# Kernel tuning notes

Hardware: AMD Instinct MI355X
Metric: run time of the kernel (lower is better)

Reference implementation:

```python
import jax, jax.numpy as jnp
import numpy as np

D_MODEL = 1024
N_HEADS = 16
N_KV_HEADS = 4
HEAD_DIM = D_MODEL // N_HEADS
NUM_REP = N_HEADS // N_KV_HEADS
B, T = 2, 2048


def setup_inputs() -> dict:
    key = jax.random.key(0)
    ks = jax.random.split(key, 9)
    s = 0.02
    x = jax.random.normal(ks[0], (B, T, D_MODEL), dtype=jnp.float32)
    # causal mask: True = masked (matches torch masked_fill semantics)
    mask = jnp.triu(jnp.ones((T, T), dtype=bool), k=1)[None, None]
    kv_dim = N_KV_HEADS * HEAD_DIM
    return {
        "x": x,
        "mask": mask,
        "Wq": jax.random.normal(ks[1], (D_MODEL, D_MODEL), jnp.float32) * s,
        "bq": jnp.zeros((D_MODEL,), jnp.float32),
        "Wk": jax.random.normal(ks[2], (D_MODEL, kv_dim), jnp.float32) * s,
        "bk": jnp.zeros((kv_dim,), jnp.float32),
        "Wv": jax.random.normal(ks[3], (D_MODEL, kv_dim), jnp.float32) * s,
        "bv": jnp.zeros((kv_dim,), jnp.float32),
        "Wo": jax.random.normal(ks[4], (D_MODEL, D_MODEL), jnp.float32) * s,
        "bo": jnp.zeros((D_MODEL,), jnp.float32),
    }


def reference(x, mask, Wq, bq, Wk, bk, Wv, bv, Wo, bo):
    Bx, Tx, C = x.shape
    # projections
    q = (x @ Wq + bq).reshape(Bx, Tx, N_HEADS, HEAD_DIM).transpose(0, 2, 1, 3)  # (B,H,T,D)
    k = (x @ Wk + bk).reshape(Bx, Tx, N_KV_HEADS, HEAD_DIM)
    v = (x @ Wv + bv).reshape(Bx, Tx, N_KV_HEADS, HEAD_DIM)
    # repeat_kv: expand+reshape == repeat along head axis
    k = jnp.repeat(k, NUM_REP, axis=2).transpose(0, 2, 1, 3)  # (B,H,T,D)
    v = jnp.repeat(v, NUM_REP, axis=2).transpose(0, 2, 1, 3)
    scale = 1.0 / jnp.sqrt(jnp.asarray(HEAD_DIM, x.dtype))
    attn = jnp.einsum('bhtd,bhsd->bhts', q, k) * scale  # (B,H,T,T)
    attn = jnp.where(mask, -jnp.inf, attn)
    attn = jax.nn.softmax(attn, axis=-1)
    out = jnp.einsum('bhts,bhsd->bhtd', attn, v)
    out = out.transpose(0, 2, 1, 3).reshape(Bx, Tx, C)
    return out @ Wo + bo
```

## Files before the change

kernel.cpp:

```cpp
#include <hip/hip_runtime.h>
#include <hip/hip_bf16.h>
#include <cmath>
#include <stdint.h>


typedef __attribute__((ext_vector_type(4))) float f32x4;
typedef __attribute__((ext_vector_type(16))) float f32x16;
typedef __attribute__((ext_vector_type(8))) short s16x8;
typedef __attribute__((ext_vector_type(8))) unsigned short u16x8;

#define MFMA32(a, b, c) __builtin_amdgcn_mfma_f32_32x32x16_bf16(a, b, c, 0, 0, 0)

__device__ __forceinline__ unsigned short f2bf(float f) {
    unsigned int u = __float_as_uint(f);
    u += 0x7FFFu + ((u >> 16) & 1u);
    return (unsigned short)(u >> 16);
}

__device__ __forceinline__ unsigned int pktr(float lo, float hi) {
    return __builtin_amdgcn_perm(__float_as_uint(hi), __float_as_uint(lo), 0x07060302u);
}

__device__ __forceinline__ void async16(void* lds, const void* g) {
    __builtin_amdgcn_global_load_lds(
        (const __attribute__((address_space(1))) unsigned int*)g,
        (__attribute__((address_space(3))) unsigned int*)lds, 16, 0, 0);
}

__global__ __launch_bounds__(256) void prep(
        const float* __restrict__ x,
        const float* __restrict__ Wq, const float* __restrict__ Wk,
        const float* __restrict__ Wv, const float* __restrict__ Wo,
        const float* __restrict__ bq, const float* __restrict__ bk,
        const float* __restrict__ bv,
        unsigned short* __restrict__ xb, unsigned short* __restrict__ Wqkv,
        unsigned short* __restrict__ Wot, float* __restrict__ biasq, float qscale) {
    __shared__ unsigned short sx[128 * 72];
    __shared__ float tile[32][33];
    const int bid = blockIdx.x, tid = threadIdx.x;
    if (bid < 512) {
        const int mt = bid >> 4, kt = bid & 15;
#pragma unroll
        for (int i = 0; i < 8; ++i) {
            const int flat = (i * 256 + tid) * 4;
            const int row = flat >> 6, col = flat & 63;
            f32x4 ld = *reinterpret_cast<const f32x4*>(
                &x[(size_t)(mt * 128 + row) * 1024 + kt * 64 + col]);
            unsigned short* d = &sx[row * 72 + col];
            d[0] = f2bf(ld.x); d[1] = f2bf(ld.y); d[2] = f2bf(ld.z); d[3] = f2bf(ld.w);
        }
        __syncthreads();
#pragma unroll
        for (int j = 0; j < 4; ++j) {
            const int idx = j * 256 + tid;
            const int kb = idx >> 7, m = idx & 127;
            u16x8 v = *reinterpret_cast<const u16x8*>(&sx[m * 72 + kb * 8]);
            *reinterpret_cast<u16x8*>(
                &xb[(size_t)(((mt * 16 + kt) * 8 + kb) * 128 + m) * 8]) = v;
        }
    } else if (bid < 3072) {
        int id = bid - 512;
        const float* W; unsigned short* out; int N, nbase; float scale = 1.0f;
        if (id < 1024)      { W = Wq; out = Wqkv; N = 1024; nbase = 0;    scale = qscale; }
        else if (id < 1280) { W = Wk; out = Wqkv; N = 256;  nbase = 1024; id -= 1024; }
        else if (id < 1536) { W = Wv; out = Wqkv; N = 256;  nbase = 1280; id -= 1280; }
        else                { W = Wo; out = Wot;  N = 1024; nbase = 0;    id -= 1536; }
        const int nb = N >> 5;
        const int n0 = (id % nb) * 32, k0 = (id / nb) * 32;
        const int tx = tid & 31, ty = tid >> 5;
#pragma unroll
        for (int r = 0; r < 4; ++r)
            tile[ty + r * 8][tx] = W[(size_t)(k0 + ty + r * 8) * N + n0 + tx];
        __syncthreads();
        const int k = k0 + tx;
#pragma unroll
        for (int r = 0; r < 4; ++r) {
            const int n = nbase + n0 + ty + r * 8;
            size_t addr = (size_t)((n >> 6) * 16 + (k >> 6)) * 4096
                        + (size_t)((((k >> 3) & 7) * 64 + (n & 63)) * 8 + (k & 7));
            out[addr] = f2bf(tile[tx][ty + r * 8] * scale);
        }
    } else {
        const int i = (bid - 3072) * 256 + tid;
        if (i < 1024) biasq[i] = bq[i] * qscale;
        else if (i < 1280) biasq[i] = bk[i - 1024];
        else biasq[i] = bv[i - 1280];
    }
}

template <int EPI>
__global__ __launch_bounds__(256) void gemm_mn(
        const unsigned short* __restrict__ A, const unsigned short* __restrict__ Bt,
        const float* __restrict__ bias,
        unsigned short* __restrict__ oQ, unsigned short* __restrict__ oK,
        unsigned short* __restrict__ oV, float* __restrict__ oF) {
    __shared__ alignas(16) unsigned short smem[24576];
    const int tid = threadIdx.x;
    const int lane = tid & 63, w = tid >> 6;
    const int l31 = lane & 31, grp = lane >> 5;
    const int m0 = blockIdx.y * 128, n0 = blockIdx.x * 64;
    const int wm = w * 32;

    const unsigned short* Abase = A + (size_t)blockIdx.y * (16 * 8192) + (size_t)tid * 8;
    const unsigned short* Bbase = Bt + (size_t)blockIdx.x * (16 * 4096) + (size_t)tid * 8;

    f32x16 acc0 = {}, acc1 = {};

#pragma unroll
    for (int i = 0; i < 4; ++i)
        async16(&smem[(size_t)(i * 256 + (tid & 192)) * 8], Abase + (size_t)i * 2048);
#pragma unroll
    for (int i = 0; i < 2; ++i)
        async16(&smem[16384 + (size_t)(i * 256 + (tid & 192)) * 8], Bbase + (size_t)i * 2048);

    for (int kt = 0; kt < 16; ++kt) {
        const int cur = kt & 1;
        unsigned short* cA = smem + cur * 8192;
        unsigned short* cB = smem + 16384 + cur * 4096;
        __syncthreads();
        if (kt < 15) {
            unsigned short* nA = smem + (cur ^ 1) * 8192;
            unsigned short* nB = smem + 16384 + (cur ^ 1) * 4096;
            const unsigned short* ab = Abase + (size_t)(kt + 1) * 8192;
            const unsigned short* bb = Bbase + (size_t)(kt + 1) * 4096;
#pragma unroll
            for (int i = 0; i < 4; ++i)
                async16(&nA[(size_t)(i * 256 + (tid & 192)) * 8], ab + (size_t)i * 2048);
#pragma unroll
            for (int i = 0; i < 2; ++i)
                async16(&nB[(size_t)(i * 256 + (tid & 192)) * 8], bb + (size_t)i * 2048);
        }
#pragma unroll
        for (int kc = 0; kc < 4; ++kc) {
            const int kb = kc * 2 + grp;
            s16x8 a  = *reinterpret_cast<const s16x8*>(&cA[(size_t)(kb * 128 + wm + l31) * 8]);
            s16x8 b0 = *reinterpret_cast<const s16x8*>(&cB[(size_t)(kb * 64 + l31) * 8]);
            s16x8 b1 = *reinterpret_cast<const s16x8*>(&cB[(size_t)(kb * 64 + 32 + l31) * 8]);
            acc0 = MFMA32(a, b0, acc0);
            acc1 = MFMA32(a, b1, acc1);
        }
    }
    const float bv0 = bias[n0 + l31], bv1 = bias[n0 + 32 + l31];
    if (EPI == 0 && n0 >= 1280) {
        __syncthreads();
#pragma unroll
        for (int r = 0; r < 16; ++r) {
            const int m = wm + (r & 3) + 8 * (r >> 2) + 4 * grp;
            smem[(size_t)l31 * 136 + m] = f2bf(acc0[r] + bv0);
            smem[(size_t)(l31 + 32) * 136 + m] = f2bf(acc1[r] + bv1);
        }
        __syncthreads();
#pragma unroll
        for (int i = 0; i < 4; ++i) {
            const int id = i * 256 + tid;
            const int n = id >> 4, mc = id & 15;
            u16x8 v = *reinterpret_cast<const u16x8*>(&smem[(size_t)n * 136 + mc * 8]);
            *reinterpret_cast<u16x8*>(&oV[(size_t)(n0 - 1280 + n) * 4096 + m0 + mc * 8]) = v;
        }
        return;
    }
#pragma unroll
    for (int r = 0; r < 16; ++r) {
        const int row = m0 + wm + (r & 3) + 8 * (r >> 2) + 4 * grp;
        const float v0 = acc0[r] + bv0, v1 = acc1[r] + bv1;
        if (EPI == 0) {
            if (n0 < 1024) {
                oQ[(size_t)row * 1024 + n0 + l31] = f2bf(v0);
                oQ[(size_t)row * 1024 + n0 + 32 + l31] = f2bf(v1);
            } else {
                oK[(size_t)row * 256 + (n0 - 1024) + l31] = f2bf(v0);
                oK[(size_t)row * 256 + (n0 - 1024) + 32 + l31] = f2bf(v1);
            }
        } else {
            oF[(size_t)row * 1024 + n0 + l31] = v0;
            oF[(size_t)row * 1024 + n0 + 32 + l31] = v1;
        }
    }
}

__global__ __launch_bounds__(512) void flash_attn(
        const unsigned short* __restrict__ Qb, const unsigned short* __restrict__ Kb,
        const unsigned short* __restrict__ Vt, unsigned short* __restrict__ Ot) {
    __shared__ alignas(16) unsigned short sK[2][64 * 72];
    __shared__ alignas(16) unsigned short sV[2][64 * 72];
    const int tid = threadIdx.x;
    const int lane = tid & 63, w = tid >> 6;
    const int ln = lane & 31, grp = lane >> 5;
    const int bh = blockIdx.x;
    const int qp = blockIdx.y;
    const int b = bh >> 4, h = bh & 15, kvh = h >> 2;
    const int myqt = (w < 4) ? qp : (15 - qp);
    const int nch_mine = 2 * myqt + 2;
    const int nch_all = 32 - 2 * qp;
    const int t0w = myqt * 128 + (w & 3) * 32;
    const int qrow_g = t0w + ln;

    const unsigned short* Qrow = Qb + (size_t)(b * 2048 + qrow_g) * 1024 + h * 64;
    s16x8 qf[4];
#pragma unroll
    for (int kk = 0; kk < 4; ++kk)
        qf[kk] = *reinterpret_cast<const s16x8*>(Qrow + kk * 16 + grp * 8);

    const unsigned short* Kbase = Kb + (size_t)(b * 2048) * 256 + kvh * 64;
    const unsigned short* Vbase = Vt + (size_t)(kvh * 64) * 4096 + (size_t)b * 2048;

    const int srow = tid >> 3, sd0 = (tid & 7) * 8;
    u16x8 kreg = *reinterpret_cast<const u16x8*>(Kbase + (size_t)srow * 256 + sd0);
    u16x8 vreg = *reinterpret_cast<const u16x8*>(Vbase + (size_t)srow * 4096 + sd0);

    f32x16 o0 = {}, o1 = {};
    float ltot = 0.f;
    s16x8 pfv[4];
    s16x8 vp0[4], vp1[4];

    for (int c = 0; c < nch_all; ++c) {
        unsigned short* bK = sK[c & 1];
        unsigned short* bV = sV[c & 1];
        *reinterpret_cast<u16x8*>(&bK[srow * 72 + sd0]) = kreg;
        *reinterpret_cast<u16x8*>(&bV[srow * 72 + sd0]) = vreg;
        __syncthreads();
        if (c + 1 < nch_all) {
            const int s1 = (c + 1) * 64;
            kreg = *reinterpret_cast<const u16x8*>(Kbase + (size_t)(s1 + srow) * 256 + sd0);
            vreg = *reinterpret_cast<const u16x8*>(Vbase + (size_t)srow * 4096 + s1 + sd0);
        }
        if (c >= 1 && c <= nch_mine) {
#pragma unroll
            for (int kkp = 0; kkp < 4; ++kkp) {
                o0 = MFMA32(pfv[kkp], vp0[kkp], o0);
                o1 = MFMA32(pfv[kkp], vp1[kkp], o1);
            }
        }
        if (c < nch_mine) {
            const int s0 = c * 64;
#pragma unroll
            for (int kkp = 0; kkp < 4; ++kkp) {
                vp0[kkp] = *reinterpret_cast<const s16x8*>(&bV[ln * 72 + kkp * 16 + grp * 8]);
                vp1[kkp] = *reinterpret_cast<const s16x8*>(&bV[(32 + ln) * 72 + kkp * 16 + grp * 8]);
            }
            f32x16 st0 = {}, st1 = {};
#pragma unroll
            for (int kk = 0; kk < 4; ++kk) {
                s16x8 k0 = *reinterpret_cast<const s16x8*>(&bK[ln * 72 + kk * 16 + grp * 8]);
                s16x8 k1 = *reinterpret_cast<const s16x8*>(&bK[(32 + ln) * 72 + kk * 16 + grp * 8]);
                st0 = MFMA32(k0, qf[kk], st0);
                st1 = MFMA32(k1, qf[kk], st1);
            }
            if (s0 + 63 > t0w) {
#pragma unroll
                for (int r = 0; r < 16; ++r) {
                    const int keyo = s0 + (r & 3) + 8 * (r >> 2) + 4 * grp;
                    if (keyo > qrow_g)      st0[r] = -INFINITY;
                    if (keyo + 32 > qrow_g) st1[r] = -INFINITY;
                }
            }
            f32x16 p0, p1;
#pragma unroll
            for (int r = 0; r < 16; ++r) {
                p0[r] = __builtin_amdgcn_exp2f(st0[r]);
                p1[r] = __builtin_amdgcn_exp2f(st1[r]);
            }
            float a0 = 0.f, a1 = 0.f, a2 = 0.f, a3 = 0.f;
#pragma unroll
            for (int r = 0; r < 16; r += 2) {
                a0 += p0[r]; a1 += p0[r + 1];
                a2 += p1[r]; a3 += p1[r + 1];
            }
            ltot += (a0 + a1) + (a2 + a3);
#pragma unroll
            for (int kkp = 0; kkp < 4; ++kkp) {
                const f32x16& pm = (kkp < 2) ? p0 : p1;
                const int A4 = 8 * (kkp & 1);
                unsigned int pA0 = pktr(pm[A4 + 0], pm[A4 + 1]);
                unsigned int pA1 = pktr(pm[A4 + 2], pm[A4 + 3]);
                unsigned int pB0 = pktr(pm[A4 + 4], pm[A4 + 5]);
                unsigned int pB1 = pktr(pm[A4 + 6], pm[A4 + 7]);
                unsigned int x0 = (unsigned int)__shfl_xor((int)(grp ? pA0 : pB0), 32, 64);
                unsigned int x1 = (unsigned int)__shfl_xor((int)(grp ? pA1 : pB1), 32, 64);
                union { unsigned int u[4]; s16x8 v; } pf;
                pf.u[0] = grp ? x0 : pA0;
                pf.u[1] = grp ? x1 : pA1;
                pf.u[2] = grp ? pB0 : x0;
                pf.u[3] = grp ? pB1 : x1;
                pfv[kkp] = pf.v;
            }
        }
    }
    if (w >= 4) {
#pragma unroll
        for (int kkp = 0; kkp < 4; ++kkp) {
            o0 = MFMA32(pfv[kkp], vp0[kkp], o0);
            o1 = MFMA32(pfv[kkp], vp1[kkp], o1);
        }
    }

    const float lfull = ltot + __shfl_xor(ltot, 32, 64);
    const float rl = 1.0f / lfull;
    unsigned short* Otb = Ot + (size_t)((b * 16 + myqt) * 16 + h) * 8192
                             + (size_t)(ln >> 3) * 1024 + (ln & 7);
#pragma unroll
    for (int r = 0; r < 16; ++r) {
        const int row = (r & 3) + 8 * (r >> 2) + 4 * grp;
        const float rr = __shfl(rl, row, 64);
        const size_t off = (size_t)((w & 3) * 32 + row) * 8;
        Otb[off]        = f2bf(o0[r] * rr);
        Otb[off + 4096] = f2bf(o1[r] * rr);
    }
}

extern "C" void kernel_launch(void* const* d_in, const int* in_sizes, int n_in,
                              void* d_out, int out_size, void* d_ws, size_t ws_size,
                              hipStream_t stream) {
    const float* x  = (const float*)d_in[0];
    const float* Wq = (const float*)d_in[2];
    const float* bq = (const float*)d_in[3];
    const float* Wk = (const float*)d_in[4];
    const float* bk = (const float*)d_in[5];
    const float* Wv = (const float*)d_in[6];
    const float* bv = (const float*)d_in[7];
    const float* Wo = (const float*)d_in[8];
    const float* bo = (const float*)d_in[9];
    float* out = (float*)d_out;

    char* ws = (char*)d_ws;
    unsigned short* xb    = (unsigned short*)(ws);
    unsigned short* Wqkv  = (unsigned short*)(ws + (8u  << 20));
    unsigned short* Wot   = (unsigned short*)(ws + (12u << 20));
    float*          biasq = (float*)         (ws + (15u << 20));
    unsigned short* Qb    = (unsigned short*)(ws + (16u << 20));
    unsigned short* Kb    = (unsigned short*)(ws + (24u << 20));
    unsigned short* Vtp   = (unsigned short*)(ws + (26u << 20));
    unsigned short* Otl   = (unsigned short*)(ws + (28u << 20));

    const float qscale = 0.125f * 1.4426950408889634f;

    prep<<<3078, 256, 0, stream>>>(x, Wq, Wk, Wv, Wo, bq, bk, bv,
                                   xb, Wqkv, Wot, biasq, qscale);
    gemm_mn<0><<<dim3(24, 32), 256, 0, stream>>>(xb, Wqkv, biasq, Qb, Kb, Vtp, nullptr);
    flash_attn<<<dim3(32, 8), 512, 0, stream>>>(Qb, Kb, Vtp, Otl);
    gemm_mn<1><<<dim3(16, 32), 256, 0, stream>>>(Otl, Wot, bo, nullptr, nullptr, nullptr, out);
}
```

Before: 168.7 us.

## Split flash attention into single-wave blocks reading K/V directly from global

Replaces the 512-thread flash attention block, which staged K/V tiles through double-buffered LDS with barriers, with 2048 single-wavefront blocks. Each block handles one 32-row query strip and loads K and V fragments straight from global memory into registers. Strips are launched longest-first, and the block index is ordered so that the four query heads sharing a KV head run close together for L2 reuse. This removes LDS traffic and __syncthreads and allows finer load balancing. The cost is that K/V reuse across waves in a block is lost, raising global/L2 load traffic, and there is no software prefetch overlapping loads with compute.

```diff
diff --git a/kernel.cpp b/kernel.cpp
--- a/kernel.cpp
+++ b/kernel.cpp
@@ -178,22 +178,19 @@
     }
 }
 
-__global__ __launch_bounds__(512) void flash_attn(
+__global__ __launch_bounds__(64) void flash_attn(
         const unsigned short* __restrict__ Qb, const unsigned short* __restrict__ Kb,
         const unsigned short* __restrict__ Vt, unsigned short* __restrict__ Ot) {
-    __shared__ alignas(16) unsigned short sK[2][64 * 72];
-    __shared__ alignas(16) unsigned short sV[2][64 * 72];
-    const int tid = threadIdx.x;
-    const int lane = tid & 63, w = tid >> 6;
+    const int lane = threadIdx.x;
     const int ln = lane & 31, grp = lane >> 5;
-    const int bh = blockIdx.x;
-    const int qp = blockIdx.y;
-    const int b = bh >> 4, h = bh & 15, kvh = h >> 2;
-    const int myqt = (w < 4) ? qp : (15 - qp);
-    const int nch_mine = 2 * myqt + 2;
-    const int nch_all = 32 - 2 * qp;
-    const int t0w = myqt * 128 + (w & 3) * 32;
+    const int id = blockIdx.x;
+    const int kvh = id & 3;
+    const int b = (id >> 2) & 1;
+    const int h = kvh * 4 + ((id >> 3) & 3);
+    const int strip = 63 - (id >> 5);
+    const int t0w = strip * 32;
     const int qrow_g = t0w + ln;
+    const int nch = (strip >> 1) + 1;
 
     const unsigned short* Qrow = Qb + (size_t)(b * 2048 + qrow_g) * 1024 + h * 64;
     s16x8 qf[4];
@@ -201,108 +198,82 @@
     for (int kk = 0; kk < 4; ++kk)
         qf[kk] = *reinterpret_cast<const s16x8*>(Qrow + kk * 16 + grp * 8);
 
-    const unsigned short* Kbase = Kb + (size_t)(b * 2048) * 256 + kvh * 64;
-    const unsigned short* Vbase = Vt + (size_t)(kvh * 64) * 4096 + (size_t)b * 2048;
-
-    const int srow = tid >> 3, sd0 = (tid & 7) * 8;
-    u16x8 kreg = *reinterpret_cast<const u16x8*>(Kbase + (size_t)srow * 256 + sd0);
-    u16x8 vreg = *reinterpret_cast<const u16x8*>(Vbase + (size_t)srow * 4096 + sd0);
+    const unsigned short* Kp = Kb + (size_t)(b * 2048) * 256 + kvh * 64;
+    const unsigned short* Vp = Vt + (size_t)(kvh * 64) * 4096 + (size_t)b * 2048;
+    const unsigned short* kr0 = Kp + (size_t)ln * 256 + grp * 8;
+    const unsigned short* kr1 = Kp + (size_t)(32 + ln) * 256 + grp * 8;
+    const unsigned short* vr0 = Vp + (size_t)ln * 4096 + grp * 8;
+    const unsigned short* vr1 = Vp + (size_t)(32 + ln) * 4096 + grp * 8;
 
     f32x16 o0 = {}, o1 = {};
     float ltot = 0.f;
-    s16x8 pfv[4];
-    s16x8 vp0[4], vp1[4];
-
-    for (int c = 0; c < nch_all; ++c) {
-        unsigned short* bK = sK[c & 1];
-        unsigned short* bV = sV[c & 1];
-        *reinterpret_cast<u16x8*>(&bK[srow * 72 + sd0]) = kreg;
-        *reinterpret_cast<u16x8*>(&bV[srow * 72 + sd0]) = vreg;
-        __syncthreads();
-        if (c + 1 < nch_all) {
-            const int s1 = (c + 1) * 64;
-            kreg = *reinterpret_cast<const u16x8*>(Kbase + (size_t)(s1 + srow) * 256 + sd0);
-            vreg = *reinterpret_cast<const u16x8*>(Vbase + (size_t)srow * 4096 + s1 + sd0);
-        }
-        if (c >= 1 && c <= nch_mine) {
-#pragma unroll
-            for (int kkp = 0; kkp < 4; ++kkp) {
-                o0 = MFMA32(pfv[kkp], vp0[kkp], o0);
-                o1 = MFMA32(pfv[kkp], vp1[kkp], o1);
+
+    for (int c = 0; c < nch; ++c) {
+        const int s0 = c * 64;
+        s16x8 kf0[4], kf1[4], vf0[4], vf1[4];
+#pragma unroll
+        for (int kk = 0; kk < 4; ++kk) {
+            kf0[kk] = *reinterpret_cast<const s16x8*>(kr0 + (size_t)s0 * 256 + kk * 16);
+            kf1[kk] = *reinterpret_cast<const s16x8*>(kr1 + (size_t)s0 * 256 + kk * 16);
+            vf0[kk] = *reinterpret_cast<const s16x8*>(vr0 + s0 + kk * 16);
+            vf1[kk] = *reinterpret_cast<const s16x8*>(vr1 + s0 + kk * 16);
+        }
+        f32x16 st0 = {}, st1 = {};
+#pragma unroll
+        for (int kk = 0; kk < 4; ++kk) {
+            st0 = MFMA32(kf0[kk], qf[kk], st0);
+            st1 = MFMA32(kf1[kk], qf[kk], st1);
+        }
+        if (s0 + 63 > t0w) {
+#pragma unroll
+            for (int r = 0; r < 16; ++r) {
+                const int keyo = s0 + (r & 3) + 8 * (r >> 2) + 4 * grp;
+                if (keyo > qrow_g)      st0[r] = -INFINITY;
+                if (keyo + 32 > qrow_g) st1[r] = -INFINITY;
             }
         }
-        if (c < nch_mine) {
-            const int s0 = c * 64;
-#pragma unroll
-            for (int kkp = 0; kkp < 4; ++kkp) {
-                vp0[kkp] = *reinterpret_cast<const s16x8*>(&bV[ln * 72 + kkp * 16 + grp * 8]);
-                vp1[kkp] = *reinterpret_cast<const s16x8*>(&bV[(32 + ln) * 72 + kkp * 16 + grp * 8]);
-            }
-            f32x16 st0 = {}, st1 = {};
-#pragma unroll
-            for (int kk = 0; kk < 4; ++kk) {
-                s16x8 k0 = *reinterpret_cast<const s16x8*>(&bK[ln * 72 + kk * 16 + grp * 8]);
-                s16x8 k1 = *reinterpret_cast<const s16x8*>(&bK[(32 + ln) * 72 + kk * 16 + grp * 8]);
-                st0 = MFMA32(k0, qf[kk], st0);
-                st1 = MFMA32(k1, qf[kk], st1);
-            }
-            if (s0 + 63 > t0w) {
-#pragma unroll
-                for (int r = 0; r < 16; ++r) {
-                    const int keyo = s0 + (r & 3) + 8 * (r >> 2) + 4 * grp;
-                    if (keyo > qrow_g)      st0[r] = -INFINITY;
-                    if (keyo + 32 > qrow_g) st1[r] = -INFINITY;
-                }
-            }
-            f32x16 p0, p1;
-#pragma unroll
-            for (int r = 0; r < 16; ++r) {
-                p0[r] = __builtin_amdgcn_exp2f(st0[r]);
-                p1[r] = __builtin_amdgcn_exp2f(st1[r]);
-            }
-            float a0 = 0.f, a1 = 0.f, a2 = 0.f, a3 = 0.f;
-#pragma unroll
-            for (int r = 0; r < 16; r += 2) {
-                a0 += p0[r]; a1 += p0[r + 1];
-                a2 += p1[r]; a3 += p1[r + 1];
-            }
-            ltot += (a0 + a1) + (a2 + a3);
-#pragma unroll
-            for (int kkp = 0; kkp < 4; ++kkp) {
-                const f32x16& pm = (kkp < 2) ? p0 : p1;
-                const int A4 = 8 * (kkp & 1);
-                unsigned int pA0 = pktr(pm[A4 + 0], pm[A4 + 1]);
-                unsigned int pA1 = pktr(pm[A4 + 2], pm[A4 + 3]);
-                unsigned int pB0 = pktr(pm[A4 + 4], pm[A4 + 5]);
-                unsigned int pB1 = pktr(pm[A4 + 6], pm[A4 + 7]);
-                unsigned int x0 = (unsigned int)__shfl_xor((int)(grp ? pA0 : pB0), 32, 64);
-                unsigned int x1 = (unsigned int)__shfl_xor((int)(grp ? pA1 : pB1), 32, 64);
-                union { unsigned int u[4]; s16x8 v; } pf;
-                pf.u[0] = grp ? x0 : pA0;
-                pf.u[1] = grp ? x1 : pA1;
-                pf.u[2] = grp ? pB0 : x0;
-                pf.u[3] = grp ? pB1 : x1;
-                pfv[kkp] = pf.v;
-            }
-        }
-    }
-    if (w >= 4) {
+        f32x16 p0, p1;
+#pragma unroll
+        for (int r = 0; r < 16; ++r) {
+            p0[r] = __builtin_amdgcn_exp2f(st0[r]);
+            p1[r] = __builtin_amdgcn_exp2f(st1[r]);
+        }
+        float a0 = 0.f, a1 = 0.f, a2 = 0.f, a3 = 0.f;
+#pragma unroll
+        for (int r = 0; r < 16; r += 2) {
+            a0 += p0[r]; a1 += p0[r + 1];
+            a2 += p1[r]; a3 += p1[r + 1];
+        }
+        ltot += (a0 + a1) + (a2 + a3);
 #pragma unroll
         for (int kkp = 0; kkp < 4; ++kkp) {
-            o0 = MFMA32(pfv[kkp], vp0[kkp], o0);
-            o1 = MFMA32(pfv[kkp], vp1[kkp], o1);
+            const f32x16& pm = (kkp < 2) ? p0 : p1;
+            const int A4 = 8 * (kkp & 1);
+            unsigned int pA0 = pktr(pm[A4 + 0], pm[A4 + 1]);
+            unsigned int pA1 = pktr(pm[A4 + 2], pm[A4 + 3]);
+            unsigned int pB0 = pktr(pm[A4 + 4], pm[A4 + 5]);
+            unsigned int pB1 = pktr(pm[A4 + 6], pm[A4 + 7]);
+            unsigned int x0 = (unsigned int)__shfl_xor((int)(grp ? pA0 : pB0), 32, 64);
+            unsigned int x1 = (unsigned int)__shfl_xor((int)(grp ? pA1 : pB1), 32, 64);
+            union { unsigned int u[4]; s16x8 v; } pf;
+            pf.u[0] = grp ? x0 : pA0;
+            pf.u[1] = grp ? x1 : pA1;
+            pf.u[2] = grp ? pB0 : x0;
+            pf.u[3] = grp ? pB1 : x1;
+            o0 = MFMA32(pf.v, vf0[kkp], o0);
+            o1 = MFMA32(pf.v, vf1[kkp], o1);
         }
     }
 
     const float lfull = ltot + __shfl_xor(ltot, 32, 64);
     const float rl = 1.0f / lfull;
-    unsigned short* Otb = Ot + (size_t)((b * 16 + myqt) * 16 + h) * 8192
+    unsigned short* Otb = Ot + (size_t)((b * 16 + (strip >> 2)) * 16 + h) * 8192
                              + (size_t)(ln >> 3) * 1024 + (ln & 7);
 #pragma unroll
     for (int r = 0; r < 16; ++r) {
         const int row = (r & 3) + 8 * (r >> 2) + 4 * grp;
         const float rr = __shfl(rl, row, 64);
-        const size_t off = (size_t)((w & 3) * 32 + row) * 8;
+        const size_t off = (size_t)((strip & 3) * 32 + row) * 8;
         Otb[off]        = f2bf(o0[r] * rr);
         Otb[off + 4096] = f2bf(o1[r] * rr);
     }
@@ -337,6 +308,6 @@
     prep<<<3078, 256, 0, stream>>>(x, Wq, Wk, Wv, Wo, bq, bk, bv,
                                    xb, Wqkv, Wot, biasq, qscale);
     gemm_mn<0><<<dim3(24, 32), 256, 0, stream>>>(xb, Wqkv, biasq, Qb, Kb, Vtp, nullptr);
-    flash_attn<<<dim3(32, 8), 512, 0, stream>>>(Qb, Kb, Vtp, Otl);
+    flash_attn<<<2048, 64, 0, stream>>>(Qb, Kb, Vtp, Otl);
     gemm_mn<1><<<dim3(16, 32), 256, 0, stream>>>(Otl, Wot, bo, nullptr, nullptr, nullptr, out);
 }
```

Result: slower. 198.1 us (+17.4%).
